# Kernel tuning notes

Measured on AMD Instinct MI355X. Metric: run time of the kernel, lower is better.

The kernel has to match this reference:

```python
import jax, jax.numpy as jnp
import numpy as np

B, T, D, H = 64, 2048, 128, 256  # batch, time, input features, num_cells


def setup_inputs() -> dict:
    key = jax.random.key(0)
    ks = jax.random.split(key, 8)
    w = lambda k, shape: (jax.random.normal(k, shape, dtype=jnp.float32) * 0.05)
    return {
        "x": jax.random.normal(ks[0], (B, T, D), dtype=jnp.float32),
        "k_fwd": w(ks[1], (D, 4 * H)),
        "r_fwd": w(ks[2], (H, 4 * H)),
        "b_fwd": jnp.zeros((4 * H,), jnp.float32),
        "k_bwd": w(ks[3], (D, 4 * H)),
        "r_bwd": w(ks[4], (H, 4 * H)),
        "b_bwd": jnp.zeros((4 * H,), jnp.float32),
        "att_w": jax.random.uniform(ks[5], (H,), dtype=jnp.float32),
    }


def _lstm(x, kernel, rec, bias):
    """Keras-style LSTM (gate order i,f,c,o), return_sequences=True. x: [B,T,D] -> [B,T,H]."""
    xw = jnp.einsum('btd,dk->btk', x, kernel) + bias  # precompute input contribution [B,T,4H]
    h0 = jnp.zeros((x.shape[0], rec.shape[0]), x.dtype)

    def step(carry, xw_t):
        h, c = carry
        z = xw_t + h @ rec  # [B,4H]
        i, f, g, o = jnp.split(z, 4, axis=-1)
        c = jax.nn.sigmoid(f) * c + jax.nn.sigmoid(i) * jnp.tanh(g)
        h = jax.nn.sigmoid(o) * jnp.tanh(c)
        return (h, c), h

    _, hs = jax.lax.scan(step, (h0, h0), jnp.swapaxes(xw, 0, 1))  # hs: [T,B,H]
    return jnp.swapaxes(hs, 0, 1)


def reference(x, k_fwd, r_fwd, b_fwd, k_bwd, r_bwd, b_bwd, att_w):
    # Bidirectional LSTM, merge_mode='sum'
    h_f = _lstm(x, k_fwd, r_fwd, b_fwd)
    h_b = _lstm(x[:, ::-1], k_bwd, r_bwd, b_bwd)[:, ::-1]
    h = h_f + h_b  # [B,T,H]
    # Additive attention pooling (dropout identity at inference)
    m = jnp.tanh(h)
    a = jax.nn.softmax(jnp.einsum('h,bth->bt', att_w, m), axis=-1)  # [B,T]
    r = jnp.einsum('bth,bt->bh', h, a)  # [B,H]
    return jnp.tanh(r)
```

## Files before the change

kernel.cpp:

```cpp
#include <hip/hip_runtime.h>
#include <cstdint>
#include <cstddef>

#define TT 2048
#define DD 128
#define HH 256
#define G4 1024

typedef _Float16 half4_t __attribute__((ext_vector_type(4)));
typedef _Float16 half8_t __attribute__((ext_vector_type(8)));
typedef float floatx4 __attribute__((ext_vector_type(4)));

union H4U64 { uint64_t u; half4_t h; };
union H8U64x2 { uint64_t u[2]; half8_t h; };

__device__ __forceinline__ float sigm(float x) { return 1.f / (1.f + __expf(-x)); }
__device__ __forceinline__ float tanh_f(float x) { return 1.f - 2.f / (1.f + __expf(2.f * x)); }

__device__ __forceinline__ half8_t cvt8(float4 a, float4 b) {
  half8_t v;
  v[0] = (_Float16)a.x; v[1] = (_Float16)a.y; v[2] = (_Float16)a.z; v[3] = (_Float16)a.w;
  v[4] = (_Float16)b.x; v[5] = (_Float16)b.y; v[6] = (_Float16)b.z; v[7] = (_Float16)b.w;
  return v;
}

__global__ void prep_kernel(const float* __restrict__ rf, const float* __restrict__ rb,
                            const float* __restrict__ kf, const float* __restrict__ kb,
                            _Float16* __restrict__ RT, _Float16* __restrict__ KT) {
  int idx = blockIdx.x * 256 + threadIdx.x;
  if (idx < 2 * G4 * HH) {
    int dir = idx >> 18, k = (idx >> 10) & 255, n = idx & 1023;
    const float* src = dir ? rb : rf;
    RT[((size_t)(dir * G4 + n)) * HH + k] = (_Float16)src[(size_t)k * G4 + n];
  } else {
    int i2 = idx - 2 * G4 * HH;
    int dir = i2 >> 17, k = (i2 >> 10) & 127, n = i2 & 1023;
    const float* src = dir ? kb : kf;
    KT[((size_t)(dir * G4 + n)) * DD + k] = (_Float16)src[(size_t)k * G4 + n];
  }
}


#define SENT 0xFFFFFFFFFFFFFFFFull

__global__ __launch_bounds__(256, 1) void lstm_rec_kernel(
    const float* __restrict__ x,
    const float* __restrict__ bias_f, const float* __restrict__ bias_b,
    const _Float16* __restrict__ RT, const _Float16* __restrict__ KT,
    uint64_t* __restrict__ ring, _Float16* __restrict__ hseq) {
  const int bid = blockIdx.x;
  const int split = bid >> 3;
  const int g = bid & 7;
  const int dir = g >> 2;
  const int bg = g & 3;
  const int tid = threadIdx.x;
  const int w = tid >> 6, lane = tid & 63;
  const int lo16 = lane & 15, q = lane >> 4;

  __shared__ _Float16 tile[2][64][20];

  const float* __restrict__ bias = dir ? bias_b : bias_f;

  half8_t bR[4][8], bK[4][4];
  float bgate[4];
#pragma unroll
  for (int gate = 0; gate < 4; ++gate) {
    const int col = gate * 256 + split * 64 + w * 16 + lo16;
    const _Float16* bp = RT + (size_t)(dir * G4 + col) * HH + q * 8;
#pragma unroll
    for (int kk = 0; kk < 8; ++kk) bR[gate][kk] = *reinterpret_cast<const half8_t*>(bp + kk * 32);
    const _Float16* kp = KT + (size_t)(dir * G4 + col) * DD + q * 8;
#pragma unroll
    for (int kx = 0; kx < 4; ++kx) bK[gate][kx] = *reinterpret_cast<const half8_t*>(kp + kx * 32);
    bgate[gate] = bias[col];
  }

  const float* __restrict__ xrow = x + ((size_t)(bg * 16 + lo16) * TT) * DD;

  const int kgl  = tid >> 5;
  const int tb   = (tid >> 1) & 15;
  const int part = tid & 1;
  const int kg_global = split * 8 + kgl;
  const int hofs = split * 64 + kgl * 8 + part * 4;
  const int myofs = (kg_global * 16 + tb) * 2 + part;

  float c[4] = {0.f, 0.f, 0.f, 0.f};

  int tx = dir ? TT - 1 : 0;
  float4 xr[8];
  {
    const float* xp = xrow + (size_t)tx * DD + q * 8;
#pragma unroll
    for (int kx = 0; kx < 4; ++kx) {
      xr[2 * kx]     = *reinterpret_cast<const float4*>(xp + kx * 32);
      xr[2 * kx + 1] = *reinterpret_cast<const float4*>(xp + kx * 32 + 4);
    }
  }
  half8_t ax[4];
#pragma unroll
  for (int kx = 0; kx < 4; ++kx) ax[kx] = cvt8(xr[2 * kx], xr[2 * kx + 1]);

  for (int s = 0; s < TT; ++s) {
    tx = dir ? (TT - 1 - s) : s;

    uint64_t g0[8], g1[8];
    const uint64_t* gp = ring;
    if (s > 0) {
      gp = ring + ((size_t)((((s - 1) & 3) * 8 + g))) * 1024 + (size_t)((q * 16 + lo16) * 2);
#pragma unroll
      for (int kk = 0; kk < 8; ++kk) {
        g0[kk] = __hip_atomic_load(gp + (size_t)kk * 128,     __ATOMIC_RELAXED, __HIP_MEMORY_SCOPE_AGENT);
        g1[kk] = __hip_atomic_load(gp + (size_t)kk * 128 + 1, __ATOMIC_RELAXED, __HIP_MEMORY_SCOPE_AGENT);
      }
    }

    {
      const int sn = (s + 1 < TT) ? s + 1 : s;
      const int txn = dir ? (TT - 1 - sn) : sn;
      const float* xp = xrow + (size_t)txn * DD + q * 8;
#pragma unroll
      for (int kx = 0; kx < 4; ++kx) {
        xr[2 * kx]     = *reinterpret_cast<const float4*>(xp + kx * 32);
        xr[2 * kx + 1] = *reinterpret_cast<const float4*>(xp + kx * 32 + 4);
      }
    }

    floatx4 acc[4];
#pragma unroll
    for (int gate = 0; gate < 4; ++gate) acc[gate] = floatx4{0.f, 0.f, 0.f, 0.f};

#pragma unroll
    for (int kx = 0; kx < 4; ++kx)
#pragma unroll
      for (int gate = 0; gate < 4; ++gate)
        acc[gate] = __builtin_amdgcn_mfma_f32_16x16x32_f16(ax[kx], bK[gate][kx], acc[gate], 0, 0, 0);

    if (s > 0) {
      while (true) {
        bool ok = true;
#pragma unroll
        for (int kk = 0; kk < 8; ++kk) ok = ok & (g0[kk] != SENT) & (g1[kk] != SENT);
        if (__all(ok)) break;
#pragma unroll
        for (int kk = 0; kk < 8; ++kk) {
          if (g0[kk] == SENT)
            g0[kk] = __hip_atomic_load(gp + (size_t)kk * 128,     __ATOMIC_RELAXED, __HIP_MEMORY_SCOPE_AGENT);
          if (g1[kk] == SENT)
            g1[kk] = __hip_atomic_load(gp + (size_t)kk * 128 + 1, __ATOMIC_RELAXED, __HIP_MEMORY_SCOPE_AGENT);
        }
      }

      __hip_atomic_store(ring + ((size_t)((((s + 2) & 3) * 8 + g))) * 1024 + myofs, SENT,
                         __ATOMIC_RELAXED, __HIP_MEMORY_SCOPE_AGENT);

#pragma unroll
      for (int kk = 0; kk < 8; ++kk) {
        H8U64x2 u;
        u.u[0] = g0[kk];
        u.u[1] = g1[kk];
#pragma unroll
        for (int gate = 0; gate < 4; ++gate)
          acc[gate] = __builtin_amdgcn_mfma_f32_16x16x32_f16(u.h, bR[gate][kk], acc[gate], 0, 0, 0);
      }
    }

    const int par = s & 1;
    {
      half4_t hv4;
#pragma unroll
      for (int r = 0; r < 4; ++r) {
        const float zi = acc[0][r] + bgate[0];
        const float zf = acc[1][r] + bgate[1];
        const float zg = acc[2][r] + bgate[2];
        const float zo = acc[3][r] + bgate[3];
        c[r] = sigm(zf) * c[r] + sigm(zi) * tanh_f(zg);
        hv4[r] = (_Float16)(sigm(zo) * tanh_f(c[r]));
      }
      *reinterpret_cast<half4_t*>(&tile[par][w * 16 + lo16][q * 4]) = hv4;
    }
    __syncthreads();

    {
      H4U64 val;
#pragma unroll
      for (int j = 0; j < 4; ++j) val.h[j] = tile[par][kgl * 8 + part * 4 + j][tb];
      asm volatile("s_waitcnt vmcnt(0)" ::: "memory");
      __hip_atomic_store(ring + ((size_t)((s & 3) * 8 + g)) * 1024 + myofs, val.u,
                         __ATOMIC_RELAXED, __HIP_MEMORY_SCOPE_AGENT);
      *reinterpret_cast<uint64_t*>(hseq + ((size_t)g * TT + tx) * (16 * HH) + (size_t)tb * HH + hofs) = val.u;
    }

#pragma unroll
    for (int kx = 0; kx < 4; ++kx) ax[kx] = cvt8(xr[2 * kx], xr[2 * kx + 1]);
  }
}


__global__ __launch_bounds__(256) void attn_kernel(const _Float16* __restrict__ h_ex,
                                                   const float* __restrict__ att_w,
                                                   float* __restrict__ out) {
  const int b = blockIdx.x;
  const int bg = b >> 4, b16 = b & 15;
  const int tid = threadIdx.x;
  const int w = tid >> 6, lane = tid & 63;
  __shared__ float sc[TT];
  __shared__ float red[8];
  const size_t ST = 16 * HH;
  const _Float16* __restrict__ hf = h_ex + (size_t)bg * TT * ST + b16 * HH;
  const _Float16* __restrict__ hb = h_ex + (size_t)(4 + bg) * TT * ST + b16 * HH;

  const int h0 = lane * 4;
  const float aw0 = att_w[h0], aw1 = att_w[h0 + 1], aw2 = att_w[h0 + 2], aw3 = att_w[h0 + 3];

  for (int t = w; t < TT; t += 4) {
    half4_t f4 = *reinterpret_cast<const half4_t*>(hf + (size_t)t * ST + h0);
    half4_t b4 = *reinterpret_cast<const half4_t*>(hb + (size_t)t * ST + h0);
    float s = aw0 * tanh_f((float)f4[0] + (float)b4[0])
            + aw1 * tanh_f((float)f4[1] + (float)b4[1])
            + aw2 * tanh_f((float)f4[2] + (float)b4[2])
            + aw3 * tanh_f((float)f4[3] + (float)b4[3]);
#pragma unroll
    for (int off = 32; off >= 1; off >>= 1) s += __shfl_xor(s, off);
    if (lane == 0) sc[t] = s;
  }
  __syncthreads();

  float m = -1e30f;
  for (int i = tid; i < TT; i += 256) m = fmaxf(m, sc[i]);
#pragma unroll
  for (int off = 32; off >= 1; off >>= 1) m = fmaxf(m, __shfl_xor(m, off));
  if (lane == 0) red[w] = m;
  __syncthreads();
  m = fmaxf(fmaxf(red[0], red[1]), fmaxf(red[2], red[3]));

  float ssum = 0.f;
  for (int i = tid; i < TT; i += 256) {
    float e = __expf(sc[i] - m);
    sc[i] = e;
    ssum += e;
  }
#pragma unroll
  for (int off = 32; off >= 1; off >>= 1) ssum += __shfl_xor(ssum, off);
  if (lane == 0) red[4 + w] = ssum;
  __syncthreads();
  const float inv = 1.f / (red[4] + red[5] + red[6] + red[7]);

  float r = 0.f;
  const _Float16* pf = hf + tid;
  const _Float16* pb = hb + tid;
  for (int t = 0; t < TT; ++t)
    r += sc[t] * ((float)pf[(size_t)t * ST] + (float)pb[(size_t)t * ST]);
  out[b * HH + tid] = tanh_f(r * inv);
}


extern "C" void kernel_launch(void* const* d_in, const int* in_sizes, int n_in,
                              void* d_out, int out_size, void* d_ws, size_t ws_size,
                              hipStream_t stream) {
  const float* x     = (const float*)d_in[0];
  const float* k_fwd = (const float*)d_in[1];
  const float* r_fwd = (const float*)d_in[2];
  const float* b_fwd = (const float*)d_in[3];
  const float* k_bwd = (const float*)d_in[4];
  const float* r_bwd = (const float*)d_in[5];
  const float* b_bwd = (const float*)d_in[6];
  const float* att_w = (const float*)d_in[7];
  float* out = (float*)d_out;

  const size_t RT_bytes   = (size_t)2 * G4 * HH * sizeof(_Float16);
  const size_t KT_bytes   = (size_t)2 * G4 * DD * sizeof(_Float16);
  const size_t ring_bytes = (size_t)4 * 8 * 1024 * sizeof(uint64_t);
  char* ws = (char*)d_ws;
  _Float16* RT    = (_Float16*)ws;
  _Float16* KT    = (_Float16*)(ws + RT_bytes);
  uint64_t* ring  = (uint64_t*)(ws + RT_bytes + KT_bytes);
  _Float16* hseq  = (_Float16*)(ws + RT_bytes + KT_bytes + ring_bytes);

  hipMemsetAsync(ring, 0xFF, ring_bytes, stream);
  hipLaunchKernelGGL(prep_kernel, dim3(3072), dim3(256), 0, stream,
                     r_fwd, r_bwd, k_fwd, k_bwd, RT, KT);
  hipLaunchKernelGGL(lstm_rec_kernel, dim3(32), dim3(256), 0, stream,
                     x, b_fwd, b_bwd, RT, KT, ring, hseq);
  hipLaunchKernelGGL(attn_kernel, dim3(64), dim3(256), 0, stream, hseq, att_w, out);
}
```

Measured before the change: 7.312 ms.

## Duplicate the cross-block hidden-state ring into fast and safe copies for polling

```diff
diff --git a/kernel.cpp b/kernel.cpp
--- a/kernel.cpp
+++ b/kernel.cpp
@@ -22,6 +22,14 @@
   v[0] = (_Float16)a.x; v[1] = (_Float16)a.y; v[2] = (_Float16)a.z; v[3] = (_Float16)a.w;
   v[4] = (_Float16)b.x; v[5] = (_Float16)b.y; v[6] = (_Float16)b.z; v[7] = (_Float16)b.w;
   return v;
+}
+
+__device__ __forceinline__ void fast_pair(const uint64_t* p, uint64_t& a, uint64_t& b) {
+  asm volatile("global_load_dwordx2 %0, %2, off sc0\n\t"
+               "global_load_dwordx2 %1, %2, off offset:8 sc0"
+               : "=&v"(a), "=&v"(b)
+               : "v"(p)
+               : "memory");
 }
 
 __global__ void prep_kernel(const float* __restrict__ rf, const float* __restrict__ rb,
@@ -47,7 +55,8 @@
     const float* __restrict__ x,
     const float* __restrict__ bias_f, const float* __restrict__ bias_b,
     const _Float16* __restrict__ RT, const _Float16* __restrict__ KT,
-    uint64_t* __restrict__ ring, _Float16* __restrict__ hseq) {
+    uint64_t* __restrict__ ringF, uint64_t* __restrict__ ringS,
+    _Float16* __restrict__ hseq) {
   const int bid = blockIdx.x;
   const int split = bid >> 3;
   const int g = bid & 7;
@@ -103,15 +112,15 @@
   for (int s = 0; s < TT; ++s) {
     tx = dir ? (TT - 1 - s) : s;
 
-    uint64_t g0[8], g1[8];
-    const uint64_t* gp = ring;
+    uint64_t f0[8], f1[8];
+    const uint64_t* gpF = ringF;
+    const uint64_t* gpS = ringS;
     if (s > 0) {
-      gp = ring + ((size_t)((((s - 1) & 3) * 8 + g))) * 1024 + (size_t)((q * 16 + lo16) * 2);
-#pragma unroll
-      for (int kk = 0; kk < 8; ++kk) {
-        g0[kk] = __hip_atomic_load(gp + (size_t)kk * 128,     __ATOMIC_RELAXED, __HIP_MEMORY_SCOPE_AGENT);
-        g1[kk] = __hip_atomic_load(gp + (size_t)kk * 128 + 1, __ATOMIC_RELAXED, __HIP_MEMORY_SCOPE_AGENT);
-      }
+      const size_t slotoff = ((size_t)(((s - 1) & 3) * 8 + g)) * 1024 + (size_t)((q * 16 + lo16) * 2);
+      gpF = ringF + slotoff;
+      gpS = ringS + slotoff;
+#pragma unroll
+      for (int kk = 0; kk < 8; ++kk) fast_pair(gpF + (size_t)kk * 128, f0[kk], f1[kk]);
     }
 
     {
@@ -136,28 +145,49 @@
         acc[gate] = __builtin_amdgcn_mfma_f32_16x16x32_f16(ax[kx], bK[gate][kx], acc[gate], 0, 0, 0);
 
     if (s > 0) {
+      asm volatile("s_waitcnt vmcnt(8)" ::: "memory");
+      __builtin_amdgcn_sched_barrier(0);
+
+      int it = 0;
       while (true) {
-        bool ok = true;
-#pragma unroll
-        for (int kk = 0; kk < 8; ++kk) ok = ok & (g0[kk] != SENT) & (g1[kk] != SENT);
-        if (__all(ok)) break;
+        bool okv = true;
+#pragma unroll
+        for (int kk = 0; kk < 8; ++kk) okv = okv & (f0[kk] != SENT) & (f1[kk] != SENT);
+        if (__all(okv)) break;
+        ++it;
+        if ((it & 3) == 0) {
+#pragma unroll
+          for (int kk = 0; kk < 8; ++kk) {
+            uint64_t a0 = __hip_atomic_load(gpS + (size_t)kk * 128,     __ATOMIC_RELAXED, __HIP_MEMORY_SCOPE_AGENT);
+            uint64_t a1 = __hip_atomic_load(gpS + (size_t)kk * 128 + 1, __ATOMIC_RELAXED, __HIP_MEMORY_SCOPE_AGENT);
+            f0[kk] = (f0[kk] != SENT) ? f0[kk] : a0;
+            f1[kk] = (f1[kk] != SENT) ? f1[kk] : a1;
+          }
+        }
+        uint64_t t0[8], t1[8];
+#pragma unroll
+        for (int kk = 0; kk < 8; ++kk) fast_pair(gpF + (size_t)kk * 128, t0[kk], t1[kk]);
+        asm volatile("s_waitcnt vmcnt(0)" ::: "memory");
+        __builtin_amdgcn_sched_barrier(0);
 #pragma unroll
         for (int kk = 0; kk < 8; ++kk) {
-          if (g0[kk] == SENT)
-            g0[kk] = __hip_atomic_load(gp + (size_t)kk * 128,     __ATOMIC_RELAXED, __HIP_MEMORY_SCOPE_AGENT);
-          if (g1[kk] == SENT)
-            g1[kk] = __hip_atomic_load(gp + (size_t)kk * 128 + 1, __ATOMIC_RELAXED, __HIP_MEMORY_SCOPE_AGENT);
+          f0[kk] = (f0[kk] != SENT) ? f0[kk] : t0[kk];
+          f1[kk] = (f1[kk] != SENT) ? f1[kk] : t1[kk];
         }
       }
 
-      __hip_atomic_store(ring + ((size_t)((((s + 2) & 3) * 8 + g))) * 1024 + myofs, SENT,
-                         __ATOMIC_RELAXED, __HIP_MEMORY_SCOPE_AGENT);
+      {
+        uint64_t* rpF = ringF + ((size_t)((((s + 2) & 3) * 8 + g))) * 1024 + myofs;
+        uint64_t* rpS = ringS + ((size_t)((((s + 2) & 3) * 8 + g))) * 1024 + myofs;
+        *rpF = SENT;
+        __hip_atomic_store(rpS, SENT, __ATOMIC_RELAXED, __HIP_MEMORY_SCOPE_AGENT);
+      }
 
 #pragma unroll
       for (int kk = 0; kk < 8; ++kk) {
         H8U64x2 u;
-        u.u[0] = g0[kk];
-        u.u[1] = g1[kk];
+        u.u[0] = f0[kk];
+        u.u[1] = f1[kk];
 #pragma unroll
         for (int gate = 0; gate < 4; ++gate)
           acc[gate] = __builtin_amdgcn_mfma_f32_16x16x32_f16(u.h, bR[gate][kk], acc[gate], 0, 0, 0);
@@ -184,9 +214,9 @@
       H4U64 val;
 #pragma unroll
       for (int j = 0; j < 4; ++j) val.h[j] = tile[par][kgl * 8 + part * 4 + j][tb];
-      asm volatile("s_waitcnt vmcnt(0)" ::: "memory");
-      __hip_atomic_store(ring + ((size_t)((s & 3) * 8 + g)) * 1024 + myofs, val.u,
-                         __ATOMIC_RELAXED, __HIP_MEMORY_SCOPE_AGENT);
+      const size_t po = ((size_t)((s & 3) * 8 + g)) * 1024 + myofs;
+      ringF[po] = val.u;
+      __hip_atomic_store(ringS + po, val.u, __ATOMIC_RELAXED, __HIP_MEMORY_SCOPE_AGENT);
       *reinterpret_cast<uint64_t*>(hseq + ((size_t)g * TT + tx) * (16 * HH) + (size_t)tb * HH + hofs) = val.u;
     }
 
@@ -273,13 +303,14 @@
   char* ws = (char*)d_ws;
   _Float16* RT    = (_Float16*)ws;
   _Float16* KT    = (_Float16*)(ws + RT_bytes);
-  uint64_t* ring  = (uint64_t*)(ws + RT_bytes + KT_bytes);
-  _Float16* hseq  = (_Float16*)(ws + RT_bytes + KT_bytes + ring_bytes);
-
-  hipMemsetAsync(ring, 0xFF, ring_bytes, stream);
+  uint64_t* ringF = (uint64_t*)(ws + RT_bytes + KT_bytes);
+  uint64_t* ringS = (uint64_t*)(ws + RT_bytes + KT_bytes + ring_bytes);
+  _Float16* hseq  = (_Float16*)(ws + RT_bytes + KT_bytes + 2 * ring_bytes);
+
+  hipMemsetAsync(ringF, 0xFF, 2 * ring_bytes, stream);
   hipLaunchKernelGGL(prep_kernel, dim3(3072), dim3(256), 0, stream,
                      r_fwd, r_bwd, k_fwd, k_bwd, RT, KT);
   hipLaunchKernelGGL(lstm_rec_kernel, dim3(32), dim3(256), 0, stream,
-                     x, b_fwd, b_bwd, RT, KT, ring, hseq);
+                     x, b_fwd, b_bwd, RT, KT, ringF, ringS, hseq);
   hipLaunchKernelGGL(attn_kernel, dim3(64), dim3(256), 0, stream, hseq, att_w, out);
 }
```

After: 10.37 ms. 1.42x slower.

## Use 512-thread blocks so half the recurrent state stays in LDS

Applied to the files above, without the earlier changes.

```diff
diff --git a/kernel.cpp b/kernel.cpp
--- a/kernel.cpp
+++ b/kernel.cpp
@@ -43,7 +43,7 @@
 
 #define SENT 0xFFFFFFFFFFFFFFFFull
 
-__global__ __launch_bounds__(256, 1) void lstm_rec_kernel(
+__global__ __launch_bounds__(512, 1) void lstm_rec_kernel(
     const float* __restrict__ x,
     const float* __restrict__ bias_f, const float* __restrict__ bias_b,
     const _Float16* __restrict__ RT, const _Float16* __restrict__ KT,
@@ -57,7 +57,7 @@
   const int w = tid >> 6, lane = tid & 63;
   const int lo16 = lane & 15, q = lane >> 4;
 
-  __shared__ _Float16 tile[2][64][20];
+  __shared__ char tileB[2 * 16 * 256];
 
   const float* __restrict__ bias = dir ? bias_b : bias_f;
 
@@ -65,7 +65,7 @@
   float bgate[4];
 #pragma unroll
   for (int gate = 0; gate < 4; ++gate) {
-    const int col = gate * 256 + split * 64 + w * 16 + lo16;
+    const int col = gate * 256 + split * 128 + w * 16 + lo16;
     const _Float16* bp = RT + (size_t)(dir * G4 + col) * HH + q * 8;
 #pragma unroll
     for (int kk = 0; kk < 8; ++kk) bR[gate][kk] = *reinterpret_cast<const half8_t*>(bp + kk * 32);
@@ -80,9 +80,11 @@
   const int kgl  = tid >> 5;
   const int tb   = (tid >> 1) & 15;
   const int part = tid & 1;
-  const int kg_global = split * 8 + kgl;
-  const int hofs = split * 64 + kgl * 8 + part * 4;
+  const int kg_global = split * 16 + kgl;
+  const int hofs = split * 128 + kgl * 8 + part * 4;
   const int myofs = (kg_global * 16 + tb) * 2 + part;
+
+  const int remote_base = (1 - split) * 512;
 
   float c[4] = {0.f, 0.f, 0.f, 0.f};
 
@@ -102,16 +104,29 @@
 
   for (int s = 0; s < TT; ++s) {
     tx = dir ? (TT - 1 - s) : s;
-
-    uint64_t g0[8], g1[8];
+    const int par = s & 1;
+    char* const wrbuf = tileB + par * 4096;
+    const char* const rdbuf = tileB + (par ^ 1) * 4096;
+
+    uint64_t g0[4], g1[4];
     const uint64_t* gp = ring;
     if (s > 0) {
-      gp = ring + ((size_t)((((s - 1) & 3) * 8 + g))) * 1024 + (size_t)((q * 16 + lo16) * 2);
-#pragma unroll
-      for (int kk = 0; kk < 8; ++kk) {
+      gp = ring + ((size_t)(((s - 1) & 3) * 8 + g)) * 1024
+               + (size_t)(remote_base + q * 32 + lo16 * 2);
+#pragma unroll
+      for (int kk = 0; kk < 4; ++kk) {
         g0[kk] = __hip_atomic_load(gp + (size_t)kk * 128,     __ATOMIC_RELAXED, __HIP_MEMORY_SCOPE_AGENT);
         g1[kk] = __hip_atomic_load(gp + (size_t)kk * 128 + 1, __ATOMIC_RELAXED, __HIP_MEMORY_SCOPE_AGENT);
       }
+    }
+
+    half8_t ah_own[4];
+    if (s > 0) {
+      const int rowb = lo16 * 256;
+      const int sw = (lo16 & 7) << 4;
+#pragma unroll
+      for (int kk = 0; kk < 4; ++kk)
+        ah_own[kk] = *reinterpret_cast<const half8_t*>(rdbuf + rowb + ((kk * 64 + q * 16) ^ sw));
     }
 
     {
@@ -136,13 +151,20 @@
         acc[gate] = __builtin_amdgcn_mfma_f32_16x16x32_f16(ax[kx], bK[gate][kx], acc[gate], 0, 0, 0);
 
     if (s > 0) {
+      const int ob = split * 4;
+#pragma unroll
+      for (int kk = 0; kk < 4; ++kk)
+#pragma unroll
+        for (int gate = 0; gate < 4; ++gate)
+          acc[gate] = __builtin_amdgcn_mfma_f32_16x16x32_f16(ah_own[kk], bR[gate][ob + kk], acc[gate], 0, 0, 0);
+
       while (true) {
         bool ok = true;
 #pragma unroll
-        for (int kk = 0; kk < 8; ++kk) ok = ok & (g0[kk] != SENT) & (g1[kk] != SENT);
+        for (int kk = 0; kk < 4; ++kk) ok = ok & (g0[kk] != SENT) & (g1[kk] != SENT);
         if (__all(ok)) break;
 #pragma unroll
-        for (int kk = 0; kk < 8; ++kk) {
+        for (int kk = 0; kk < 4; ++kk) {
           if (g0[kk] == SENT)
             g0[kk] = __hip_atomic_load(gp + (size_t)kk * 128,     __ATOMIC_RELAXED, __HIP_MEMORY_SCOPE_AGENT);
           if (g1[kk] == SENT)
@@ -153,20 +175,20 @@
       __hip_atomic_store(ring + ((size_t)((((s + 2) & 3) * 8 + g))) * 1024 + myofs, SENT,
                          __ATOMIC_RELAXED, __HIP_MEMORY_SCOPE_AGENT);
 
-#pragma unroll
-      for (int kk = 0; kk < 8; ++kk) {
+      const int rb4 = (1 - split) * 4;
+#pragma unroll
+      for (int kk = 0; kk < 4; ++kk) {
         H8U64x2 u;
         u.u[0] = g0[kk];
         u.u[1] = g1[kk];
 #pragma unroll
         for (int gate = 0; gate < 4; ++gate)
-          acc[gate] = __builtin_amdgcn_mfma_f32_16x16x32_f16(u.h, bR[gate][kk], acc[gate], 0, 0, 0);
-      }
-    }
-
-    const int par = s & 1;
+          acc[gate] = __builtin_amdgcn_mfma_f32_16x16x32_f16(u.h, bR[gate][rb4 + kk], acc[gate], 0, 0, 0);
+      }
+    }
+
     {
-      half4_t hv4;
+      const int lh2 = (w * 16 + lo16) * 2;
 #pragma unroll
       for (int r = 0; r < 4; ++r) {
         const float zi = acc[0][r] + bgate[0];
@@ -174,20 +196,20 @@
         const float zg = acc[2][r] + bgate[2];
         const float zo = acc[3][r] + bgate[3];
         c[r] = sigm(zf) * c[r] + sigm(zi) * tanh_f(zg);
-        hv4[r] = (_Float16)(sigm(zo) * tanh_f(c[r]));
-      }
-      *reinterpret_cast<half4_t*>(&tile[par][w * 16 + lo16][q * 4]) = hv4;
+        const _Float16 hv = (_Float16)(sigm(zo) * tanh_f(c[r]));
+        const int b = q * 4 + r;
+        *reinterpret_cast<_Float16*>(wrbuf + b * 256 + (lh2 ^ ((b & 7) << 4))) = hv;
+      }
     }
     __syncthreads();
 
     {
-      H4U64 val;
-#pragma unroll
-      for (int j = 0; j < 4; ++j) val.h[j] = tile[par][kgl * 8 + part * 4 + j][tb];
+      const uint64_t val = *reinterpret_cast<const uint64_t*>(
+          wrbuf + tb * 256 + ((kgl * 16 + part * 8) ^ ((tb & 7) << 4)));
       asm volatile("s_waitcnt vmcnt(0)" ::: "memory");
-      __hip_atomic_store(ring + ((size_t)((s & 3) * 8 + g)) * 1024 + myofs, val.u,
+      __hip_atomic_store(ring + ((size_t)((s & 3) * 8 + g)) * 1024 + myofs, val,
                          __ATOMIC_RELAXED, __HIP_MEMORY_SCOPE_AGENT);
-      *reinterpret_cast<uint64_t*>(hseq + ((size_t)g * TT + tx) * (16 * HH) + (size_t)tb * HH + hofs) = val.u;
+      *reinterpret_cast<uint64_t*>(hseq + ((size_t)g * TT + tx) * (16 * HH) + (size_t)tb * HH + hofs) = val;
     }
 
 #pragma unroll
@@ -279,7 +301,7 @@
   hipMemsetAsync(ring, 0xFF, ring_bytes, stream);
   hipLaunchKernelGGL(prep_kernel, dim3(3072), dim3(256), 0, stream,
                      r_fwd, r_bwd, k_fwd, k_bwd, RT, KT);
-  hipLaunchKernelGGL(lstm_rec_kernel, dim3(32), dim3(256), 0, stream,
+  hipLaunchKernelGGL(lstm_rec_kernel, dim3(16), dim3(512), 0, stream,
                      x, b_fwd, b_bwd, RT, KT, ring, hseq);
   hipLaunchKernelGGL(attn_kernel, dim3(64), dim3(256), 0, stream, hseq, att_w, out);
 }
```

Result: slower. 23.24 ms (+217.8%).
